# Kernel tuning notes

Measured on AMD Instinct MI355X. Metric: run time of the kernel, lower is better.

The kernel has to match this reference:

```python
import jax, jax.numpy as jnp
import numpy as np

T, B, H, W_IMG = 8, 4, 128, 128
NUM_CLS = 21
LEAK = 0.99   # config.leak_mem
THR = 1.0     # config.def_threshold
EPS = 1e-4    # BatchNorm2d eps


@jax.custom_vjp
def spike(mem):
    # Heaviside spike with 'Linear' surrogate gradient
    return (mem > THR).astype(mem.dtype)

def _spike_fwd(mem):
    return spike(mem), mem

def _spike_bwd(mem, g):
    # triangular (linear) surrogate around threshold
    return (g * jnp.maximum(0.0, 1.0 - jnp.abs(mem - THR)),)

spike.defvjp(_spike_fwd, _spike_bwd)


def conv(x, w, pad, dil=1):
    return jax.lax.conv_general_dilated(
        x, w, window_strides=(1, 1), padding=[(pad, pad), (pad, pad)],
        rhs_dilation=(dil, dil), dimension_numbers=('NCHW', 'OIHW', 'NCHW'))


def bn_apply(x, bn_t):
    # bn_t: [3, C] = (gamma, running_mean, running_var); bias=None in the model
    g, mu, var = bn_t[0], bn_t[1], bn_t[2]
    inv = (g / jnp.sqrt(var + EPS))[None, :, None, None]
    return (x - mu[None, :, None, None]) * inv


def avgpool(x):
    # AvgPool2d(kernel=3, stride=2, padding=1), count_include_pad=True -> /9
    s = jax.lax.reduce_window(x, 0.0, jax.lax.add, (1, 1, 3, 3), (1, 1, 2, 2),
                              [(0, 0), (0, 0), (1, 1), (1, 1)])
    return s / 9.0


def lif(x, w, bn_t, mem, pad, dil=1):
    # mem = leak*mem + BN_t(conv(x)); spike; soft reset by threshold
    out = bn_apply(conv(x, w, pad, dil), bn_t)
    mem = LEAK * mem + out
    s = spike(mem)
    return mem - THR * s, s


def _forward(x, u, W0, W1, W2, W3, W4, W5, W6, W7, W8,
             bn0, bn1, bn2, bn3, bn4, bn5, bn6, bn7):
    # Poisson generator: spike when u <= |x|, carrying sign of x. [T,B,3,H,W]
    spk_in = jnp.where(u <= jnp.abs(x)[None], jnp.sign(x)[None], 0.0)
    z = lambda c, h: jnp.zeros((B, c, h, h), x.dtype)
    init = (z(64, 128), z(64, 128), z(128, 64), z(128, 64),
            z(256, 32), z(256, 32), z(256, 32), z(1024, 32), z(NUM_CLS, 32))

    def step(carry, xs):
        m0, m1, m2, m3, m4, m5, m6, m7, macc = carry
        sp, b0, b1, b2, b3, b4, b5, b6, b7 = xs
        m0, o = lif(sp, W0, b0, m0, 1)
        m1, o = lif(o, W1, b1, m1, 1)
        o = avgpool(o)                      # 128 -> 64
        m2, o = lif(o, W2, b2, m2, 1)
        m3, o = lif(o, W3, b3, m3, 1)
        o = avgpool(o)                      # 64 -> 32
        m4, o = lif(o, W4, b4, m4, 1)
        m5, o = lif(o, W5, b5, m5, 2, 2)    # atrous256
        m6, o = lif(o, W6, b6, m6, 2, 2)    # atrous256
        m7, o = lif(o, W7, b7, m7, 12, 12)  # classifier atrous1024
        macc = macc + conv(o, W8, 0)        # output layer accumulates voltage
        return (m0, m1, m2, m3, m4, m5, m6, m7, macc), None

    carry, _ = jax.lax.scan(step, init, (spk_in, bn0, bn1, bn2, bn3, bn4, bn5, bn6, bn7))
    return carry[-1] / T


def setup_inputs() -> dict:
    key = jax.random.key(0)
    ks = jax.random.split(key, 24)

    def w(k, shape):
        fan_in = int(np.prod(shape[1:]))
        return jax.random.normal(k, shape, jnp.float32) / np.sqrt(fan_in)

    def bn(k, c):
        return jax.random.uniform(k, (T, 3, c), jnp.float32, 0.25, 1.25)

    inp = {
        'x': jax.random.normal(ks[0], (B, 3, H, W_IMG), jnp.float32),
        'u': jax.random.uniform(ks[1], (T, B, 3, H, W_IMG), jnp.float32),
        'W0': w(ks[2], (64, 3, 3, 3)),
        'W1': w(ks[3], (64, 64, 3, 3)),
        'W2': w(ks[4], (128, 64, 3, 3)),
        'W3': w(ks[5], (128, 128, 3, 3)),
        'W4': w(ks[6], (256, 128, 3, 3)),
        'W5': w(ks[7], (256, 256, 3, 3)),
        'W6': w(ks[8], (256, 256, 3, 3)),
        'W7': w(ks[9], (1024, 256, 3, 3)),
        'W8': w(ks[10], (NUM_CLS, 1024, 1, 1)),
        'bn0': bn(ks[11], 64), 'bn1': bn(ks[12], 64),
        'bn2': bn(ks[13], 128), 'bn3': bn(ks[14], 128),
        'bn4': bn(ks[15], 256), 'bn5': bn(ks[16], 256),
        'bn6': bn(ks[17], 256), 'bn7': bn(ks[18], 1024),
    }
    return inp


def reference(x, u, W0, W1, W2, W3, W4, W5, W6, W7, W8,
              bn0, bn1, bn2, bn3, bn4, bn5, bn6, bn7):
    return _forward(x, u, W0, W1, W2, W3, W4, W5, W6, W7, W8,
                    bn0, bn1, bn2, bn3, bn4, bn5, bn6, bn7)
```

## Files before the change

kernel.cpp:

```cpp
#include <hip/hip_runtime.h>
#include <hip/hip_bf16.h>
#include <cstddef>
#include <cstdint>

#define LEAK  0.99f
#define THRS  1.0f
#define BNEPS 1e-4f

static constexpr int TT   = 8;
static constexpr int BB   = 4;
static constexpr int NCLS = 21;

typedef __attribute__((ext_vector_type(8))) short short8v;
typedef __attribute__((ext_vector_type(4))) float f32x4;

__global__ void zero_f32(float* __restrict__ p, int n) {
  int i = blockIdx.x * blockDim.x + threadIdx.x;
  int stride = gridDim.x * blockDim.x;
  for (; i < n; i += stride) p[i] = 0.0f;
}

__global__ void scale_f32(float* __restrict__ p, int n, float s) {
  int i = blockIdx.x * blockDim.x + threadIdx.x;
  if (i < n) p[i] *= s;
}

__global__ void wsplit(const float* __restrict__ Wsrc,
                       __hip_bfloat16* __restrict__ whi, __hip_bfloat16* __restrict__ wlo,
                       int Co, int Ci, int Cip, float scale) {
  const int Kpad = 9 * Cip;
  const int n = Co * Kpad;
  int i = blockIdx.x * 256 + threadIdx.x;
  if (i >= n) return;
  int co = i / Kpad, k = i - co * Kpad;
  int tap = k / Cip, ci = k - tap * Cip;
  float w = 0.0f;
  if (ci < Ci) w = Wsrc[((size_t)co * Ci + ci) * 9 + tap] * scale;
  __hip_bfloat16 h = __float2bfloat16(w);
  float r = w - __bfloat162float(h);
  whi[i] = h;
  wlo[i] = __float2bfloat16(r);
}

__global__ void spike_gen(const float* __restrict__ x, const float* __restrict__ u,
                          __hip_bfloat16* __restrict__ spk) {
  const int HW = 128 * 128;
  int i = blockIdx.x * 256 + threadIdx.x;
  if (i >= BB * HW) return;
  int b = i / HW, hw = i - b * HW;
#pragma unroll
  for (int c = 0; c < 3; ++c) {
    float xv = x[((size_t)b * 3 + c) * HW + hw];
    float uv = u[((size_t)b * 3 + c) * HW + hw];
    float ax = fabsf(xv);
    float sg = (xv > 0.0f) ? 1.0f : ((xv < 0.0f) ? -1.0f : 0.0f);
    float s  = (uv <= ax) ? sg : 0.0f;
    spk[(size_t)i * 32 + c] = __float2bfloat16(s);
  }
}

template<int M, int N, int GRP, int CPT, int SPLIT>
__global__ __launch_bounds__(SPLIT * 256, 4) void gemm_lif(
    const __hip_bfloat16* __restrict__ actin,
    const __hip_bfloat16* __restrict__ wsp,
    const float* __restrict__ bnt,
    float* __restrict__ mem, __hip_bfloat16* __restrict__ actout,
    const __hip_bfloat16* __restrict__ zp,
    int Co, int lgHW, int lgW, int dil, int lgGX) {
  constexpr int NW = 4;
  constexpr int Cip = CPT * 32;
  constexpr int Kpad = 9 * Cip;
  constexpr int lgcpt = (CPT == 1) ? 0 : (CPT == 2) ? 1 : (CPT == 4) ? 2 : 3;
  constexpr int R  = N * 32;
  constexpr int lgR = (N == 1) ? 5 : ((N == 2) ? 6 : 7);
  constexpr int BUFROWS = GRP * R;
  constexpr int BUFELEM = BUFROWS * 32;
  constexpr int INSTS = BUFROWS / (16 * NW);
  constexpr int AM = M * GRP;
  constexpr int WAITN = AM;
  constexpr int NCH = (9 * CPT) / SPLIT;
  constexpr int NGRP = NCH / GRP;
  static_assert(NCH % GRP == 0, "group must divide per-half chunk count");
  __shared__ __hip_bfloat16 lds[SPLIT * 2 * BUFELEM];

  const int HW = 1 << lgHW, H = HW >> lgW, W = 1 << lgW;
  const unsigned CoKpad = (unsigned)Co * Kpad;
  const int lane = threadIdx.x & 63, wid = threadIdx.x >> 6;
  const int kw = wid >> 2;
  const int wq = wid & 3;
  const int l15 = lane & 15, g = lane >> 4;
  __hip_bfloat16* ldsh = lds + kw * 2 * BUFELEM;

  const int nb = gridDim.x;
  const int flat = blockIdx.x;
  const int swz = (flat & 7) * (nb >> 3) + (flat >> 3);
  const int bx = swz & ((1 << lgGX) - 1);
  const int by = swz >> lgGX;
  const int p0  = (bx * NW + wq) * (M * 16);
  const int co0 = by * (N * 16);

  int b_[M], y_[M], x_[M];
#pragma unroll
  for (int m = 0; m < M; ++m) {
    int pb = p0 + m * 16;
    b_[m] = pb >> lgHW;
    int rem = pb & (HW - 1);
    y_[m] = rem >> lgW;
    x_[m] = (rem & (W - 1)) + l15;
  }

  const unsigned kbase = (unsigned)kw * (NCH * 32);
  unsigned sgb[INSTS];
#pragma unroll
  for (int i = 0; i < INSTS; ++i) {
    int f  = wq * (BUFROWS / NW) + i * 16 + (lane >> 2);
    int cc = f >> lgR;
    int r  = f & (R - 1);
    int half = r >> (lgR - 1);
    int co   = r & (16 * N - 1);
    int slot = (lane & 3) ^ ((co >> 1) & 3);
    sgb[i] = (unsigned)half * CoKpad + (unsigned)(co0 + co) * Kpad + slot * 8
           + cc * 32 + kbase;
  }

  auto stage = [&](int gl, int buf) {
#pragma unroll
    for (int i = 0; i < INSTS; ++i) {
      const __hip_bfloat16* gp = wsp + sgb[i] + gl * (GRP * 32);
      __hip_bfloat16* lp = &ldsh[buf * BUFELEM + (wq * (BUFROWS / NW) + i * 16) * 32];
      __builtin_amdgcn_global_load_lds(
          (const __attribute__((address_space(1))) void*)gp,
          (__attribute__((address_space(3))) void*)lp, 16, 0, 0);
    }
  };

  const __hip_bfloat16* apc[M];
  auto mkaddr = [&](int tap) {
    int ty = (tap * 11) >> 5;
    int tx = tap - ty * 3;
    int dy = (ty - 1) * dil, dx = (tx - 1) * dil;
#pragma unroll
    for (int m = 0; m < M; ++m) {
      int sy = y_[m] + dy, sx = x_[m] + dx;
      bool v = (sy >= 0) & (sy < H) & (sx >= 0) & (sx < W);
      int pix = (b_[m] << lgHW) + (sy << lgW) + sx;
      apc[m] = v ? (actin + (size_t)pix * Cip + 8 * g) : (zp + 8 * g);
    }
  };

  auto prefA_slice = [&](int cg, int cc, short8v (&dst)[GRP][M], bool force) {
    if ((cg & (CPT - 1)) == 0 || force) mkaddr(cg >> lgcpt);
    int kc = (cg & (CPT - 1)) << 5;
#pragma unroll
    for (int m = 0; m < M; ++m)
      dst[cc][m] = *(const short8v*)(apc[m] + kc);
  };

  f32x4 acc[M][N] = {};
  const int rdb = l15 * 32 + ((g ^ ((l15 >> 1) & 3)) * 8);

  short8v aA[GRP][M], aB[GRP][M];

  auto grp_body = [&](int gi, short8v (&aU)[GRP][M], short8v (&aF)[GRP][M]) {
    asm volatile("s_waitcnt vmcnt(%0)" :: "n"(WAITN) : "memory");
    __builtin_amdgcn_s_barrier();
    __builtin_amdgcn_sched_barrier(0);

    const bool more = (gi + 1 < NGRP);
    if (more) stage(gi + 1, (gi + 1) & 1);

    const __hip_bfloat16* bp = &ldsh[(gi & 1) * BUFELEM];
#pragma unroll
    for (int cc = 0; cc < GRP; ++cc) {
      if (more) prefA_slice(kw * NCH + (gi + 1) * GRP + cc, cc, aF, false);
      short8v bh[N], bl[N];
#pragma unroll
      for (int j = 0; j < N; ++j) {
        bh[j] = *(const short8v*)(bp + cc * (R * 32) + j * 512 + rdb);
        bl[j] = *(const short8v*)(bp + cc * (R * 32) + (N * 512) + j * 512 + rdb);
      }
      __builtin_amdgcn_s_setprio(1);
#pragma unroll
      for (int j = 0; j < N; ++j)
#pragma unroll
        for (int m = 0; m < M; ++m) {
          acc[m][j] = __builtin_amdgcn_mfma_f32_16x16x32_bf16(aU[cc][m], bh[j], acc[m][j], 0, 0, 0);
          acc[m][j] = __builtin_amdgcn_mfma_f32_16x16x32_bf16(aU[cc][m], bl[j], acc[m][j], 0, 0, 0);
        }
      __builtin_amdgcn_s_setprio(0);
    }
  };

  stage(0, 0);
#pragma unroll
  for (int cc = 0; cc < GRP; ++cc)
    prefA_slice(kw * NCH + cc, cc, aA, cc == 0);

#pragma unroll
  for (int gi = 0; gi < NGRP; ++gi) {
    if (gi & 1) grp_body(gi, aB, aA);
    else        grp_body(gi, aA, aB);
  }

  if constexpr (SPLIT == 2) {
    asm volatile("s_waitcnt vmcnt(0) lgkmcnt(0)" ::: "memory");
    __builtin_amdgcn_s_barrier();
    float* red = (float*)lds;
    const int tid = wq * 64 + lane;
    if (kw == 1) {
#pragma unroll
      for (int m = 0; m < M; ++m)
#pragma unroll
        for (int j = 0; j < N; ++j)
#pragma unroll
          for (int r = 0; r < 4; ++r)
            red[((m * N + j) * 4 + r) * 256 + tid] = acc[m][j][r];
    }
    asm volatile("s_waitcnt lgkmcnt(0)" ::: "memory");
    __builtin_amdgcn_s_barrier();
    if (kw == 1) return;
#pragma unroll
    for (int m = 0; m < M; ++m)
#pragma unroll
      for (int j = 0; j < N; ++j)
#pragma unroll
        for (int r = 0; r < 4; ++r)
          acc[m][j][r] += red[((m * N + j) * 4 + r) * 256 + tid];
  }

#pragma unroll
  for (int j = 0; j < N; ++j) {
    int c = co0 + j * 16 + l15;
    float ga = bnt[c], mu = bnt[Co + c], va = bnt[2 * Co + c];
    float sc = ga / sqrtf(va + BNEPS);
#pragma unroll
    for (int m = 0; m < M; ++m) {
      int pixb = p0 + m * 16 + 4 * g;
#pragma unroll
      for (int r = 0; r < 4; ++r) {
        size_t idx = (size_t)(pixb + r) * Co + c;
        float bno = (acc[m][j][r] - mu) * sc;
        float mv = LEAK * mem[idx] + bno;
        float s = (mv > THRS) ? 1.0f : 0.0f;
        actout[idx] = __float2bfloat16(s);
        mem[idx] = mv - s;
      }
    }
  }
}

__global__ void avgpool_sum8(const __hip_bfloat16* __restrict__ in,
                             __hip_bfloat16* __restrict__ out, int C, int H, int W) {
  const int Ho = H >> 1, Wo = W >> 1;
  const int C8 = C >> 3;
  const int n = BB * Ho * Wo * C8;
  int i = blockIdx.x * 256 + threadIdx.x;
  if (i >= n) return;
  int c8 = i % C8; int t = i / C8;
  int xo = t % Wo; t /= Wo;
  int yo = t % Ho; int b = t / Ho;
  const int y0 = 2 * yo - 1, x0 = 2 * xo - 1;
  float s[8] = {0, 0, 0, 0, 0, 0, 0, 0};
#pragma unroll
  for (int dy = 0; dy < 3; ++dy) {
    int iy = y0 + dy;
    if (iy < 0 || iy >= H) continue;
#pragma unroll
    for (int dx = 0; dx < 3; ++dx) {
      int ix = x0 + dx;
      if (ix < 0 || ix >= W) continue;
      short8v v = *(const short8v*)(in + (((size_t)b * H + iy) * W + ix) * C + c8 * 8);
#pragma unroll
      for (int e = 0; e < 8; ++e) {
        __hip_bfloat16_raw raw; raw.x = (unsigned short)v[e];
        s[e] += __bfloat162float(__hip_bfloat16(raw));
      }
    }
  }
  short8v o;
#pragma unroll
  for (int e = 0; e < 8; ++e) {
    __hip_bfloat16_raw raw = __hip_bfloat16_raw(__float2bfloat16(s[e]));
    o[e] = (short)raw.x;
  }
  *(short8v*)(out + (size_t)i * 8) = o;
}

__global__ void out_conv(const __hip_bfloat16* __restrict__ act,
                         const float* __restrict__ W8, float* __restrict__ out) {
  int gw = (blockIdx.x * 256 + threadIdx.x) >> 6;
  int lane = threadIdx.x & 63;
  int b = gw >> 10, pix = gw & 1023;
  const __hip_bfloat16* ap = act + ((size_t)gw << 10);
  float acc[NCLS];
#pragma unroll
  for (int c = 0; c < NCLS; ++c) acc[c] = 0.0f;
  for (int j = 0; j < 16; ++j) {
    int ci = j * 64 + lane;
    float av = __bfloat162float(ap[ci]);
#pragma unroll
    for (int c = 0; c < NCLS; ++c) acc[c] = fmaf(av, W8[c * 1024 + ci], acc[c]);
  }
#pragma unroll
  for (int c = 0; c < NCLS; ++c) {
    float v = acc[c];
    for (int off = 32; off; off >>= 1) v += __shfl_xor(v, off, 64);
    if (lane == 0) out[((size_t)b * NCLS + c) * 1024 + pix] += v;
  }
}

extern "C" void kernel_launch(void* const* d_in, const int* in_sizes, int n_in,
                              void* d_out, int out_size, void* d_ws, size_t ws_size,
                              hipStream_t stream) {
  const float* x = (const float*)d_in[0];
  const float* u = (const float*)d_in[1];
  const float* Wc[9];
  for (int i = 0; i < 9; ++i) Wc[i] = (const float*)d_in[2 + i];
  const float* bn[8];
  for (int i = 0; i < 8; ++i) bn[i] = (const float*)d_in[11 + i];

  const int Ci_[8]  = {3, 64, 64, 128, 128, 256, 256, 256};
  const int Cip_[8] = {32, 64, 64, 128, 128, 256, 256, 256};
  const int Co_[8]  = {64, 64, 128, 128, 256, 256, 256, 1024};
  const int HH_[8]  = {128, 128, 64, 64, 32, 32, 32, 32};
  const float wsc_[8] = {1.f, 1.f, 1.f / 9.f, 1.f, 1.f / 9.f, 1.f, 1.f, 1.f};

  float* ws = (float*)d_ws;
  size_t off = 0;
  auto align8 = [](size_t v) { return (v + 7) & ~(size_t)7; };

  float* memp[8];
  for (int i = 0; i < 8; ++i) {
    memp[i] = ws + off;
    off += (size_t)BB * HH_[i] * HH_[i] * Co_[i];
  }
  __hip_bfloat16* spk = (__hip_bfloat16*)(ws + off);
  off += (size_t)BB * 16384 * 32 / 2;
  __hip_bfloat16* zp = (__hip_bfloat16*)(ws + off);
  off += 256;
  const size_t zero_floats = off;
  __hip_bfloat16* actA = (__hip_bfloat16*)(ws + off); off += 2097152;
  __hip_bfloat16* actB = (__hip_bfloat16*)(ws + off); off += 2097152;
  __hip_bfloat16* wall[8];
  for (int i = 0; i < 8; ++i) {
    size_t n = (size_t)Co_[i] * 9 * Cip_[i];
    wall[i] = (__hip_bfloat16*)(ws + off);
    off = align8(off + n);
  }

  zero_f32<<<2048, 256, 0, stream>>>(ws, (int)zero_floats);
  zero_f32<<<(BB * NCLS * 1024 + 255) / 256, 256, 0, stream>>>((float*)d_out, BB * NCLS * 1024);

  for (int i = 0; i < 8; ++i) {
    int n = Co_[i] * 9 * Cip_[i];
    wsplit<<<(n + 255) / 256, 256, 0, stream>>>(Wc[i], wall[i], wall[i] + n,
                                                Co_[i], Ci_[i], Cip_[i], wsc_[i]);
  }

  const size_t uT = (size_t)BB * 3 * 16384;
  for (int t = 0; t < TT; ++t) {
    spike_gen<<<(BB * 16384 + 255) / 256, 256, 0, stream>>>(x, u + (size_t)t * uT, spk);
    gemm_lif<2, 2, 3, 1, 1><<<1024, 256, 0, stream>>>(spk,  wall[0], bn[0] + (size_t)t * 3 * 64,   memp[0], actA, zp, 64,   14, 7, 1, 9);
    gemm_lif<2, 2, 3, 2, 1><<<1024, 256, 0, stream>>>(actA, wall[1], bn[1] + (size_t)t * 3 * 64,   memp[1], actB, zp, 64,   14, 7, 1, 9);
    avgpool_sum8<<<(BB * 64 * 64 * 8 + 255) / 256, 256, 0, stream>>>(actB, actA, 64, 128, 128);
    gemm_lif<2, 2, 3, 2, 2><<<512, 512, 0, stream>>>(actA, wall[2], bn[2] + (size_t)t * 3 * 128,  memp[2], actB, zp, 128,  12, 6, 1, 7);
    gemm_lif<2, 2, 3, 4, 2><<<512, 512, 0, stream>>>(actB, wall[3], bn[3] + (size_t)t * 3 * 128,  memp[3], actA, zp, 128,  12, 6, 1, 7);
    avgpool_sum8<<<(BB * 32 * 32 * 16 + 255) / 256, 256, 0, stream>>>(actA, actB, 128, 64, 64);
    gemm_lif<1, 2, 3, 4, 2><<<512, 512, 0, stream>>>(actB, wall[4], bn[4] + (size_t)t * 3 * 256,   memp[4], actA, zp, 256,  10, 5, 1, 6);
    gemm_lif<1, 2, 4, 8, 2><<<512, 512, 0, stream>>>(actA, wall[5], bn[5] + (size_t)t * 3 * 256,   memp[5], actB, zp, 256,  10, 5, 2, 6);
    gemm_lif<1, 2, 4, 8, 2><<<512, 512, 0, stream>>>(actB, wall[6], bn[6] + (size_t)t * 3 * 256,   memp[6], actA, zp, 256,  10, 5, 2, 6);
    gemm_lif<2, 4, 2, 8, 2><<<512, 512, 0, stream>>>(actA, wall[7], bn[7] + (size_t)t * 3 * 1024, memp[7], actB, zp, 1024, 10, 5, 12, 5);
    out_conv<<<dim3(BB * 1024 / 4), 256, 0, stream>>>(actB, Wc[8], (float*)d_out);
  }
  scale_f32<<<(BB * NCLS * 1024 + 255) / 256, 256, 0, stream>>>((float*)d_out, BB * NCLS * 1024, 1.0f / TT);
}
```

Baseline: 1.948 ms.

## Pack first-layer conv taps into compact K and add specialized layer-0 kernel

Layer 0 has only 3 input channels but was padded to 32 channels per tap, which wasted MFMA work and memory traffic. The change stores spikes with 8 channels per pixel and packs 4 taps per 32-wide MFMA K slice, giving 96 K elements instead of 288. A dedicated kernel loads these packed weights into LDS asynchronously and does the conv and LIF update in 3 K-chunks. It also shrinks the spike buffer and moves it out of the zeroed region, which relies on padding lanes 3..7 being written as zero on every call.

```diff
diff --git a/kernel.cpp b/kernel.cpp
--- a/kernel.cpp
+++ b/kernel.cpp
@@ -42,12 +42,27 @@
   wlo[i] = __float2bfloat16(r);
 }
 
-__global__ void spike_gen(const float* __restrict__ x, const float* __restrict__ u,
-                          __hip_bfloat16* __restrict__ spk) {
+__global__ void wsplit_l0(const float* __restrict__ W0,
+                          __hip_bfloat16* __restrict__ whi, __hip_bfloat16* __restrict__ wlo) {
+  int i = blockIdx.x * 256 + threadIdx.x;
+  if (i >= 64 * 96) return;
+  int co = i / 96, k = i - co * 96;
+  int slot = k >> 3, ci = k & 7;
+  float w = 0.0f;
+  if (slot < 9 && ci < 3) w = W0[((size_t)co * 3 + ci) * 9 + slot];
+  __hip_bfloat16 h = __float2bfloat16(w);
+  float r = w - __bfloat162float(h);
+  whi[i] = h;
+  wlo[i] = __float2bfloat16(r);
+}
+
+__global__ void spike_gen8(const float* __restrict__ x, const float* __restrict__ u,
+                           __hip_bfloat16* __restrict__ spk) {
   const int HW = 128 * 128;
   int i = blockIdx.x * 256 + threadIdx.x;
   if (i >= BB * HW) return;
   int b = i / HW, hw = i - b * HW;
+  short8v o = {};
 #pragma unroll
   for (int c = 0; c < 3; ++c) {
     float xv = x[((size_t)b * 3 + c) * HW + hw];
@@ -55,7 +70,120 @@
     float ax = fabsf(xv);
     float sg = (xv > 0.0f) ? 1.0f : ((xv < 0.0f) ? -1.0f : 0.0f);
     float s  = (uv <= ax) ? sg : 0.0f;
-    spk[(size_t)i * 32 + c] = __float2bfloat16(s);
+    __hip_bfloat16_raw raw = __hip_bfloat16_raw(__float2bfloat16(s));
+    o[c] = (short)raw.x;
+  }
+  *(short8v*)(spk + (size_t)i * 8) = o;
+}
+
+__global__ __launch_bounds__(256) void gemm_lif_l0(
+    const __hip_bfloat16* __restrict__ spk,
+    const __hip_bfloat16* __restrict__ wsp,
+    const float* __restrict__ bnt, float* __restrict__ mem,
+    __hip_bfloat16* __restrict__ actout,
+    const __hip_bfloat16* __restrict__ zp) {
+  constexpr int M = 2, Co = 64, Kpk = 96, HW = 16384, H = 128, W = 128;
+  __shared__ __hip_bfloat16 lds[3 * 64 * 32];
+  const int lane = threadIdx.x & 63, wid = threadIdx.x >> 6;
+  const int l15 = lane & 15, g = lane >> 4;
+
+  const int nb = gridDim.x;
+  const int flat = blockIdx.x;
+  const int swz = (flat & 7) * (nb >> 3) + (flat >> 3);
+  const int bx = swz & 511, by = swz >> 9;
+  const int p0 = (bx * 4 + wid) * 32;
+  const int co0 = by * 32;
+
+  int b_[M], y_[M], x_[M];
+#pragma unroll
+  for (int m = 0; m < M; ++m) {
+    int pb = p0 + m * 16;
+    b_[m] = pb >> 14;
+    int rem = pb & (HW - 1);
+    y_[m] = rem >> 7;
+    x_[m] = (rem & 127) + l15;
+  }
+
+  unsigned sgb[3];
+#pragma unroll
+  for (int i = 0; i < 3; ++i) {
+    int f = wid * 48 + i * 16 + (lane >> 2);
+    int cc = f >> 6;
+    int r  = f & 63;
+    int half = r >> 5;
+    int co   = r & 31;
+    int slot = (lane & 3) ^ ((co >> 1) & 3);
+    sgb[i] = (unsigned)half * Co * Kpk + (unsigned)(co0 + co) * Kpk + slot * 8 + cc * 32;
+  }
+#pragma unroll
+  for (int i = 0; i < 3; ++i) {
+    const __hip_bfloat16* gp = wsp + sgb[i];
+    __hip_bfloat16* lp = &lds[(wid * 48 + i * 16) * 32];
+    __builtin_amdgcn_global_load_lds(
+        (const __attribute__((address_space(1))) void*)gp,
+        (__attribute__((address_space(3))) void*)lp, 16, 0, 0);
+  }
+
+  short8v aA[3][M];
+#pragma unroll
+  for (int c = 0; c < 3; ++c) {
+    int tap = c * 4 + g;
+    int ty = (tap * 11) >> 5;
+    int tx = tap - ty * 3;
+    int dy = ty - 1, dx = tx - 1;
+#pragma unroll
+    for (int m = 0; m < M; ++m) {
+      int sy = y_[m] + dy, sx = x_[m] + dx;
+      bool v = (tap < 9) & (sy >= 0) & (sy < H) & (sx >= 0) & (sx < W);
+      int pix = (b_[m] << 14) + (sy << 7) + sx;
+      const __hip_bfloat16* ap = v ? (spk + (size_t)pix * 8) : zp;
+      aA[c][m] = *(const short8v*)ap;
+    }
+  }
+
+  asm volatile("s_waitcnt vmcnt(%0)" :: "n"(6) : "memory");
+  __builtin_amdgcn_s_barrier();
+  __builtin_amdgcn_sched_barrier(0);
+
+  f32x4 acc[M][2] = {};
+  const int rdb = l15 * 32 + ((g ^ ((l15 >> 1) & 3)) * 8);
+#pragma unroll
+  for (int c = 0; c < 3; ++c) {
+    short8v bh[2], bl[2];
+#pragma unroll
+    for (int j = 0; j < 2; ++j) {
+      bh[j] = *(const short8v*)(&lds[c * 2048] + j * 512 + rdb);
+      bl[j] = *(const short8v*)(&lds[c * 2048] + 1024 + j * 512 + rdb);
+    }
+    __builtin_amdgcn_s_setprio(1);
+#pragma unroll
+    for (int j = 0; j < 2; ++j)
+#pragma unroll
+      for (int m = 0; m < M; ++m) {
+        acc[m][j] = __builtin_amdgcn_mfma_f32_16x16x32_bf16(aA[c][m], bh[j], acc[m][j], 0, 0, 0);
+        acc[m][j] = __builtin_amdgcn_mfma_f32_16x16x32_bf16(aA[c][m], bl[j], acc[m][j], 0, 0, 0);
+      }
+    __builtin_amdgcn_s_setprio(0);
+  }
+
+#pragma unroll
+  for (int j = 0; j < 2; ++j) {
+    int c = co0 + j * 16 + l15;
+    float ga = bnt[c], mu = bnt[Co + c], va = bnt[2 * Co + c];
+    float sc = ga / sqrtf(va + BNEPS);
+#pragma unroll
+    for (int m = 0; m < M; ++m) {
+      int pixb = p0 + m * 16 + 4 * g;
+#pragma unroll
+      for (int r = 0; r < 4; ++r) {
+        size_t idx = (size_t)(pixb + r) * Co + c;
+        float bno = (acc[m][j][r] - mu) * sc;
+        float mv = LEAK * mem[idx] + bno;
+        float s = (mv > THRS) ? 1.0f : 0.0f;
+        actout[idx] = __float2bfloat16(s);
+        mem[idx] = mv - s;
+      }
+    }
   }
 }
 
@@ -320,7 +448,7 @@
   for (int i = 0; i < 8; ++i) bn[i] = (const float*)d_in[11 + i];
 
   const int Ci_[8]  = {3, 64, 64, 128, 128, 256, 256, 256};
-  const int Cip_[8] = {32, 64, 64, 128, 128, 256, 256, 256};
+  const int Cip_[8] = {8, 64, 64, 128, 128, 256, 256, 256};
   const int Co_[8]  = {64, 64, 128, 128, 256, 256, 256, 1024};
   const int HH_[8]  = {128, 128, 64, 64, 32, 32, 32, 32};
   const float wsc_[8] = {1.f, 1.f, 1.f / 9.f, 1.f, 1.f / 9.f, 1.f, 1.f, 1.f};
@@ -334,15 +462,17 @@
     memp[i] = ws + off;
     off += (size_t)BB * HH_[i] * HH_[i] * Co_[i];
   }
-  __hip_bfloat16* spk = (__hip_bfloat16*)(ws + off);
-  off += (size_t)BB * 16384 * 32 / 2;
   __hip_bfloat16* zp = (__hip_bfloat16*)(ws + off);
   off += 256;
   const size_t zero_floats = off;
+  __hip_bfloat16* spk = (__hip_bfloat16*)(ws + off);
+  off += (size_t)BB * 16384 * 8 / 2;
   __hip_bfloat16* actA = (__hip_bfloat16*)(ws + off); off += 2097152;
   __hip_bfloat16* actB = (__hip_bfloat16*)(ws + off); off += 2097152;
   __hip_bfloat16* wall[8];
-  for (int i = 0; i < 8; ++i) {
+  wall[0] = (__hip_bfloat16*)(ws + off);
+  off = align8(off + (size_t)64 * 96);
+  for (int i = 1; i < 8; ++i) {
     size_t n = (size_t)Co_[i] * 9 * Cip_[i];
     wall[i] = (__hip_bfloat16*)(ws + off);
     off = align8(off + n);
@@ -351,7 +481,8 @@
   zero_f32<<<2048, 256, 0, stream>>>(ws, (int)zero_floats);
   zero_f32<<<(BB * NCLS * 1024 + 255) / 256, 256, 0, stream>>>((float*)d_out, BB * NCLS * 1024);
 
-  for (int i = 0; i < 8; ++i) {
+  wsplit_l0<<<(64 * 96 + 255) / 256, 256, 0, stream>>>(Wc[0], wall[0], wall[0] + 64 * 96);
+  for (int i = 1; i < 8; ++i) {
     int n = Co_[i] * 9 * Cip_[i];
     wsplit<<<(n + 255) / 256, 256, 0, stream>>>(Wc[i], wall[i], wall[i] + n,
                                                 Co_[i], Ci_[i], Cip_[i], wsc_[i]);
@@ -359,8 +490,8 @@
 
   const size_t uT = (size_t)BB * 3 * 16384;
   for (int t = 0; t < TT; ++t) {
-    spike_gen<<<(BB * 16384 + 255) / 256, 256, 0, stream>>>(x, u + (size_t)t * uT, spk);
-    gemm_lif<2, 2, 3, 1, 1><<<1024, 256, 0, stream>>>(spk,  wall[0], bn[0] + (size_t)t * 3 * 64,   memp[0], actA, zp, 64,   14, 7, 1, 9);
+    spike_gen8<<<(BB * 16384 + 255) / 256, 256, 0, stream>>>(x, u + (size_t)t * uT, spk);
+    gemm_lif_l0<<<1024, 256, 0, stream>>>(spk, wall[0], bn[0] + (size_t)t * 3 * 64, memp[0], actA, zp);
     gemm_lif<2, 2, 3, 2, 1><<<1024, 256, 0, stream>>>(actA, wall[1], bn[1] + (size_t)t * 3 * 64,   memp[1], actB, zp, 64,   14, 7, 1, 9);
     avgpool_sum8<<<(BB * 64 * 64 * 8 + 255) / 256, 256, 0, stream>>>(actB, actA, 64, 128, 128);
     gemm_lif<2, 2, 3, 2, 2><<<512, 512, 0, stream>>>(actA, wall[2], bn[2] + (size_t)t * 3 * 128,  memp[2], actB, zp, 128,  12, 6, 1, 7);
```

Result: faster. 1.908 ms (-2.0%).
